# Kernel tuning notes

Measured on AMD Instinct MI355X. Metric: run time of the kernel, lower is better.

The kernel has to match this reference:

```python
import jax, jax.numpy as jnp
import numpy as np
from jax import lax

B, T, EMB = 16384, 50, 16
NS, ND, V = 8, 8, 100000
NEXP = 4
DNN_DIM = ND + NS * EMB + EMB + EMB + EMB  # 184
NEG_INF = float(-2**32 + 1)


def setup_inputs() -> dict:
    key = jax.random.key(0)
    ks = iter(jax.random.split(key, 40))
    def p(shape, s=0.05):
        return jax.random.normal(next(ks), shape, dtype=jnp.float32) * s
    inp = {
        'dense_inputs': jax.random.normal(next(ks), (B, ND), dtype=jnp.float32),
        'sparse_tables': p((NS, V, EMB)),
        'seq_table': p((V, EMB)),
        # DIN attention MLP: input dim 4*EMB = 64
        'att_w1': p((4 * EMB, 64)), 'att_b1': jnp.zeros((64,), jnp.float32),
        'att_w2': p((64, 32)),      'att_b2': jnp.zeros((32,), jnp.float32),
        'att_w3': p((32, 1)),       'att_b3': jnp.zeros((1,), jnp.float32),
        # GRU (reset_after=True, keras default): W [EMB,3H], U [H,3H], b [2,3H]
        'gru_W': p((EMB, 3 * EMB)), 'gru_U': p((EMB, 3 * EMB)),
        'gru_b': jnp.zeros((2, 3 * EMB), jnp.float32),
        # MMOE experts (stacked over expert axis)
        'ew1': p((NEXP, DNN_DIM, 128)), 'eb1': jnp.zeros((NEXP, 128), jnp.float32),
        'ew2': p((NEXP, 128, 64)),      'eb2': jnp.zeros((NEXP, 64), jnp.float32),
        'gfw': p((DNN_DIM, NEXP)), 'gfb': jnp.zeros((NEXP,), jnp.float32),
        'glw': p((DNN_DIM, NEXP)), 'glb': jnp.zeros((NEXP,), jnp.float32),
        'fw': p((64, 1)), 'fb': jnp.zeros((1,), jnp.float32),
        'lw': p((64, 1)), 'lb': jnp.zeros((1,), jnp.float32),
        'sparse_inputs': jax.random.randint(next(ks), (B, NS), 0, V, dtype=jnp.int32),
        'seq_input': jax.random.randint(next(ks), (B, T), 0, V, dtype=jnp.int32),
        'hist_input': jax.random.randint(next(ks), (B, T), 0, V, dtype=jnp.int32),
    }
    return inp


def _din_attention(query, keys, mask, w1, b1, w2, b2, w3, b3):
    # query [B,E], keys [B,T,E], mask [B,T] float (1 valid / 0 pad)
    q = jnp.broadcast_to(query[:, None, :], keys.shape)
    att_in = jnp.concatenate([q, keys, q - keys, q * keys], axis=-1)  # [B,T,4E]
    h = jax.nn.relu(att_in @ w1 + b1)
    h = jax.nn.relu(h @ w2 + b2)
    scores = (h @ w3 + b3)[..., 0]  # [B,T]
    scores = jnp.where(mask > 0, scores, NEG_INF)
    w = jax.nn.softmax(scores, axis=1)
    return jnp.sum(w[..., None] * keys, axis=1)  # [B,E]


def _gru(x, mask_bool, W, U, b):
    # x [B,T,E], mask_bool [B,T]; keras GRU reset_after=True, masked steps keep state
    b_i, b_r = b[0], b[1]
    x_all = x @ W + b_i  # [B,T,3H]
    def step(h, inp):
        x_t, m_t = inp  # [B,3H], [B]
        rec = h @ U + b_r
        xz, xr, xh = jnp.split(x_t, 3, axis=-1)
        rz, rr, rh = jnp.split(rec, 3, axis=-1)
        z = jax.nn.sigmoid(xz + rz)
        r = jax.nn.sigmoid(xr + rr)
        hh = jnp.tanh(xh + r * rh)
        h_new = z * h + (1.0 - z) * hh
        h = jnp.where(m_t[:, None], h_new, h)
        return h, None
    h0 = jnp.zeros((x.shape[0], U.shape[0]), x.dtype)
    h, _ = lax.scan(step, h0, (x_all.transpose(1, 0, 2), mask_bool.T))
    return h  # [B,H]


def reference(dense_inputs, sparse_tables, seq_table,
              att_w1, att_b1, att_w2, att_b2, att_w3, att_b3,
              gru_W, gru_U, gru_b,
              ew1, eb1, ew2, eb2, gfw, gfb, glw, glb, fw, fb, lw, lb,
              sparse_inputs, seq_input, hist_input):
    # sparse embeddings: [B, NS, E]
    sparse_embeds = jax.vmap(lambda t, idx: t[idx], in_axes=(0, 1), out_axes=1)(
        sparse_tables, sparse_inputs)
    sparse_flat = sparse_embeds.reshape(sparse_embeds.shape[0], -1)

    # seq feature: mean pool over time
    seq_flat = jnp.mean(seq_table[seq_input], axis=1)  # [B,E]

    # history: embeds via target item table (s0), DIN attention + GRU
    hist_emb = sparse_tables[0][hist_input]            # [B,T,E]
    mask_f = (hist_input != 0).astype(jnp.float32)
    target_emb = sparse_tables[0][sparse_inputs[:, 0]]  # [B,E]
    din_out = _din_attention(target_emb, hist_emb, mask_f,
                             att_w1, att_b1, att_w2, att_b2, att_w3, att_b3)
    gru_out = _gru(hist_emb, hist_input != 0, gru_W, gru_U, gru_b)

    dnn_input = jnp.concatenate(
        [dense_inputs, sparse_flat, seq_flat, din_out, gru_out], axis=-1)  # [B,184]

    # MMOE experts (dropout is identity at inference)
    h1 = jax.nn.relu(jnp.einsum('bd,edh->beh', dnn_input, ew1) + eb1)
    h2 = jax.nn.relu(jnp.einsum('beh,eho->beo', h1, ew2) + eb2)  # [B,NEXP,64]

    gate_f = jax.nn.softmax(dnn_input @ gfw + gfb, axis=-1)  # [B,NEXP]
    gate_l = jax.nn.softmax(dnn_input @ glw + glb, axis=-1)
    fin_in = jnp.einsum('be,beo->bo', gate_f, h2)
    lik_in = jnp.einsum('be,beo->bo', gate_l, h2)

    finish = jax.nn.sigmoid(fin_in @ fw + fb)  # [B,1]
    like = jax.nn.sigmoid(lik_in @ lw + lb)    # [B,1]
    return finish, like
```

## Files before the change

kernel.cpp:

```cpp
#include <hip/hip_runtime.h>

#define BB 16384
#define TT 50
#define EMBD 16
#define NSP 8
#define NDD 8
#define VV 100000
#define DNN 184
#define NEGINF (-4294967295.0f)

typedef float f32x4 __attribute__((ext_vector_type(4)));
typedef short bf16x8 __attribute__((ext_vector_type(8)));

__device__ __forceinline__ float sigmoidf_(float x) { return 1.0f / (1.0f + __expf(-x)); }
__device__ __forceinline__ float tanhf_(float x) { return 1.0f - 2.0f / (__expf(2.0f * x) + 1.0f); }

__device__ __forceinline__ unsigned short f2bf(float x) {
    union { float f; unsigned u; } c; c.f = x;
    unsigned r = c.u + 0x7FFFu + ((c.u >> 16) & 1u);
    return (unsigned short)(r >> 16);
}
__device__ __forceinline__ unsigned pack2(float lo, float hi) {
    return (unsigned)f2bf(lo) | ((unsigned)f2bf(hi) << 16);
}

__global__ __launch_bounds__(128, 3) void k1_fused(
    const float* __restrict__ dense,
    const float* __restrict__ tables,
    const float* __restrict__ seq_table,
    const float* __restrict__ aw1, const float* __restrict__ ab1,
    const float* __restrict__ aw2, const float* __restrict__ ab2,
    const float* __restrict__ aw3, const float* __restrict__ ab3,
    const float* __restrict__ gW, const float* __restrict__ gU, const float* __restrict__ gB,
    const int* __restrict__ sparse_in, const int* __restrict__ seq_in, const int* __restrict__ hist_in,
    float* __restrict__ dnn_out)
{
    const int w = threadIdx.x >> 6;
    const int lane = threadIdx.x & 63;
    const int b = blockIdx.x * 2 + w;
    const int g = lane >> 4, r16 = lane & 15;

    __shared__ __align__(16) float histE[2][64][16];
    __shared__ float maskL[2][64];
    __shared__ float qsh[2][16];
    __shared__ float dnnL[2][DNN];
    __shared__ float wsoft[2][64];
    __shared__ __align__(16) unsigned short attB[2][64][72];

    if (lane < TT) {
        int hidx = hist_in[b * TT + lane];
        const float4* src = (const float4*)(tables + (size_t)hidx * EMBD);
        float4 a0 = src[0], a1 = src[1], a2 = src[2], a3 = src[3];
        *(float4*)&histE[w][lane][0]  = a0;
        *(float4*)&histE[w][lane][4]  = a1;
        *(float4*)&histE[w][lane][8]  = a2;
        *(float4*)&histE[w][lane][12] = a3;
        maskL[w][lane] = (hidx != 0) ? 1.0f : 0.0f;
    } else {
        float4 z = make_float4(0.f, 0.f, 0.f, 0.f);
        *(float4*)&histE[w][lane][0]  = z;
        *(float4*)&histE[w][lane][4]  = z;
        *(float4*)&histE[w][lane][8]  = z;
        *(float4*)&histE[w][lane][12] = z;
        maskL[w][lane] = 0.0f;
    }
    if (lane < EMBD) {
        int ti = sparse_in[b * NSP];
        qsh[w][lane] = tables[(size_t)ti * EMBD + lane];
    }
    if (lane < NDD) dnnL[w][lane] = dense[b * NDD + lane];
    for (int i = lane; i < NSP * EMBD; i += 64) {
        int s = i >> 4, j = i & 15;
        int idx = sparse_in[b * NSP + s];
        dnnL[w][NDD + i] = tables[((size_t)s * VV + idx) * EMBD + j];
    }
    {
        int gg = lane >> 4, j = lane & 15;
        float acc = 0.0f;
        for (int t = gg; t < TT; t += 4) {
            int idx = seq_in[b * TT + t];
            acc += seq_table[(size_t)idx * EMBD + j];
        }
        acc += __shfl_xor(acc, 16);
        acc += __shfl_xor(acc, 32);
        if (lane < EMBD) dnnL[w][NDD + NSP * EMBD + lane] = acc * (1.0f / TT);
    }
    __syncthreads();

    bf16x8 a1f[4][2];
    #pragma unroll
    for (int mt = 0; mt < 4; ++mt)
        #pragma unroll
        for (int kc = 0; kc < 2; ++kc)
            #pragma unroll
            for (int j = 0; j < 8; ++j)
                a1f[mt][kc][j] = (short)f2bf(aw1[(kc * 32 + g * 8 + j) * 64 + mt * 16 + r16]);
    bf16x8 a2f[2][2];
    #pragma unroll
    for (int mt = 0; mt < 2; ++mt)
        #pragma unroll
        for (int kc = 0; kc < 2; ++kc)
            #pragma unroll
            for (int j = 0; j < 8; ++j)
                a2f[mt][kc][j] = (short)f2bf(aw2[(kc * 32 + g * 8 + j) * 32 + mt * 16 + r16]);

    {
        float qv[16], kv[16];
        #pragma unroll
        for (int j = 0; j < 16; ++j) { qv[j] = qsh[w][j]; kv[j] = histE[w][lane][j]; }
        unsigned short* rowp = &attB[w][lane][0];
        uint4 u;
        u.x = pack2(qv[0], qv[1]);   u.y = pack2(qv[2], qv[3]);
        u.z = pack2(qv[4], qv[5]);   u.w = pack2(qv[6], qv[7]);
        *(uint4*)&rowp[0] = u;
        u.x = pack2(qv[8], qv[9]);   u.y = pack2(qv[10], qv[11]);
        u.z = pack2(qv[12], qv[13]); u.w = pack2(qv[14], qv[15]);
        *(uint4*)&rowp[8] = u;
        u.x = pack2(kv[0], kv[1]);   u.y = pack2(kv[2], kv[3]);
        u.z = pack2(kv[4], kv[5]);   u.w = pack2(kv[6], kv[7]);
        *(uint4*)&rowp[16] = u;
        u.x = pack2(kv[8], kv[9]);   u.y = pack2(kv[10], kv[11]);
        u.z = pack2(kv[12], kv[13]); u.w = pack2(kv[14], kv[15]);
        *(uint4*)&rowp[24] = u;
        u.x = pack2(qv[0]-kv[0], qv[1]-kv[1]);   u.y = pack2(qv[2]-kv[2], qv[3]-kv[3]);
        u.z = pack2(qv[4]-kv[4], qv[5]-kv[5]);   u.w = pack2(qv[6]-kv[6], qv[7]-kv[7]);
        *(uint4*)&rowp[32] = u;
        u.x = pack2(qv[8]-kv[8], qv[9]-kv[9]);   u.y = pack2(qv[10]-kv[10], qv[11]-kv[11]);
        u.z = pack2(qv[12]-kv[12], qv[13]-kv[13]); u.w = pack2(qv[14]-kv[14], qv[15]-kv[15]);
        *(uint4*)&rowp[40] = u;
        u.x = pack2(qv[0]*kv[0], qv[1]*kv[1]);   u.y = pack2(qv[2]*kv[2], qv[3]*kv[3]);
        u.z = pack2(qv[4]*kv[4], qv[5]*kv[5]);   u.w = pack2(qv[6]*kv[6], qv[7]*kv[7]);
        *(uint4*)&rowp[48] = u;
        u.x = pack2(qv[8]*kv[8], qv[9]*kv[9]);   u.y = pack2(qv[10]*kv[10], qv[11]*kv[11]);
        u.z = pack2(qv[12]*kv[12], qv[13]*kv[13]); u.w = pack2(qv[14]*kv[14], qv[15]*kv[15]);
        *(uint4*)&rowp[56] = u;
    }
    __syncthreads();

    #pragma unroll
    for (int nt = 0; nt < 4; ++nt) {
        const unsigned short* rp = &attB[w][nt * 16 + r16][g * 8];
        bf16x8 b0 = *(const bf16x8*)(rp);
        bf16x8 b1 = *(const bf16x8*)(rp + 32);
        #pragma unroll
        for (int mt = 0; mt < 4; ++mt) {
            f32x4 acc = {0.f, 0.f, 0.f, 0.f};
            acc = __builtin_amdgcn_mfma_f32_16x16x32_bf16(a1f[mt][0], b0, acc, 0, 0, 0);
            acc = __builtin_amdgcn_mfma_f32_16x16x32_bf16(a1f[mt][1], b1, acc, 0, 0, 0);
            const float4 bia = *(const float4*)(ab1 + mt * 16 + g * 4);
            float v0 = fmaxf(acc[0] + bia.x, 0.0f);
            float v1 = fmaxf(acc[1] + bia.y, 0.0f);
            float v2 = fmaxf(acc[2] + bia.z, 0.0f);
            float v3 = fmaxf(acc[3] + bia.w, 0.0f);
            uint2 pw; pw.x = pack2(v0, v1); pw.y = pack2(v2, v3);
            *(uint2*)&attB[w][nt * 16 + r16][mt * 16 + g * 4] = pw;
        }
    }

    float snt[4];
    #pragma unroll
    for (int nt = 0; nt < 4; ++nt) {
        const unsigned short* rp = &attB[w][nt * 16 + r16][g * 8];
        bf16x8 c0 = *(const bf16x8*)(rp);
        bf16x8 c1 = *(const bf16x8*)(rp + 32);
        float sp = 0.0f;
        #pragma unroll
        for (int mt = 0; mt < 2; ++mt) {
            f32x4 acc = {0.f, 0.f, 0.f, 0.f};
            acc = __builtin_amdgcn_mfma_f32_16x16x32_bf16(a2f[mt][0], c0, acc, 0, 0, 0);
            acc = __builtin_amdgcn_mfma_f32_16x16x32_bf16(a2f[mt][1], c1, acc, 0, 0, 0);
            const float4 bia = *(const float4*)(ab2 + mt * 16 + g * 4);
            const float4 w3v = *(const float4*)(aw3 + mt * 16 + g * 4);
            sp += fmaxf(acc[0] + bia.x, 0.0f) * w3v.x;
            sp += fmaxf(acc[1] + bia.y, 0.0f) * w3v.y;
            sp += fmaxf(acc[2] + bia.z, 0.0f) * w3v.z;
            sp += fmaxf(acc[3] + bia.w, 0.0f) * w3v.w;
        }
        sp += __shfl_xor(sp, 16);
        sp += __shfl_xor(sp, 32);
        snt[nt] = sp;
    }
    float score = (g == 0) ? snt[0] : (g == 1) ? snt[1] : (g == 2) ? snt[2] : snt[3];
    score += ab3[0];

    float mask = maskL[w][lane];
    score = (lane < TT && mask > 0.0f) ? score : NEGINF;
    float m = score;
    #pragma unroll
    for (int off = 32; off > 0; off >>= 1) m = fmaxf(m, __shfl_xor(m, off));
    float e = (lane < TT) ? __expf(score - m) : 0.0f;
    float ssum = e;
    #pragma unroll
    for (int off = 32; off > 0; off >>= 1) ssum += __shfl_xor(ssum, off);
    wsoft[w][lane] = e / ssum;
    __syncthreads();

    {
        float da = 0.0f;
        for (int t = g; t < TT; t += 4) da += wsoft[w][t] * histE[w][t][r16];
        da += __shfl_xor(da, 16);
        da += __shfl_xor(da, 32);
        if (lane < EMBD) dnnL[w][NDD + NSP * EMBD + EMBD + lane] = da;
    }

    float Wc[EMBD], Uc[EMBD], bi = 0.0f, br = 0.0f;
    if (lane < 48) {
        #pragma unroll
        for (int v = 0; v < EMBD; ++v) { Wc[v] = gW[v * 48 + lane]; Uc[v] = gU[v * 48 + lane]; }
        bi = gB[lane]; br = gB[48 + lane];
    }
    float hcur = 0.0f;
    for (int t = 0; t < TT; ++t) {
        float4 x0 = *(const float4*)&histE[w][t][0];
        float4 x1 = *(const float4*)&histE[w][t][4];
        float4 x2 = *(const float4*)&histE[w][t][8];
        float4 x3 = *(const float4*)&histE[w][t][12];
        float mt = maskL[w][t];
        float hv[16];
        #pragma unroll
        for (int v = 0; v < 16; ++v) hv[v] = __shfl(hcur, v);
        float xa = bi, rc = br;
        xa += x0.x*Wc[0] + x0.y*Wc[1] + x0.z*Wc[2] + x0.w*Wc[3];
        xa += x1.x*Wc[4] + x1.y*Wc[5] + x1.z*Wc[6] + x1.w*Wc[7];
        xa += x2.x*Wc[8] + x2.y*Wc[9] + x2.z*Wc[10] + x2.w*Wc[11];
        xa += x3.x*Wc[12] + x3.y*Wc[13] + x3.z*Wc[14] + x3.w*Wc[15];
        #pragma unroll
        for (int v = 0; v < 16; ++v) rc += hv[v] * Uc[v];
        float xr = __shfl(xa, lane + 16), xh = __shfl(xa, lane + 32);
        float rr = __shfl(rc, lane + 16), rh = __shfl(rc, lane + 32);
        float z  = sigmoidf_(xa + rc);
        float r  = sigmoidf_(xr + rr);
        float hh = tanhf_(xh + r * rh);
        float hnew = z * hcur + (1.0f - z) * hh;
        hcur = (mt > 0.0f) ? hnew : hcur;
    }
    if (lane < EMBD) dnnL[w][DNN - EMBD + lane] = hcur;
    __syncthreads();

    for (int i = lane; i < DNN; i += 64)
        dnn_out[(size_t)b * DNN + i] = dnnL[w][i];
}

#define BBT 8
__global__ __launch_bounds__(256) void k2_mmoe(
    const float* __restrict__ dnn_in,
    const float* __restrict__ ew1, const float* __restrict__ eb1,
    const float* __restrict__ ew2, const float* __restrict__ eb2,
    const float* __restrict__ gfw, const float* __restrict__ gfb,
    const float* __restrict__ glw, const float* __restrict__ glb,
    const float* __restrict__ fw, const float* __restrict__ fb,
    const float* __restrict__ lw, const float* __restrict__ lb,
    float* __restrict__ out)
{
    const int tid = threadIdx.x;
    const int b0 = blockIdx.x * BBT;

    __shared__ float dlds[BBT * DNN];
    __shared__ float h1L[BBT][512];
    __shared__ float h2L[BBT][256];
    __shared__ float gateL[BBT][8];

    {
        const float* drow = dnn_in + (size_t)b0 * DNN;
        for (int i = tid; i < BBT * DNN; i += 256) dlds[i] = drow[i];
    }
    __syncthreads();

    {
        int col0 = tid;
        int e0 = col0 >> 7, i0 = col0 & 127;
        const float* wp0 = ew1 + (size_t)e0 * DNN * 128 + i0;
        const float* wp1 = ew1 + (size_t)(e0 + 2) * DNN * 128 + i0;
        float acc0[BBT], acc1[BBT];
        float bias0 = eb1[col0], bias1 = eb1[col0 + 256];
        #pragma unroll
        for (int bb = 0; bb < BBT; ++bb) { acc0[bb] = bias0; acc1[bb] = bias1; }
        for (int d = 0; d < DNN; d += 4) {
            float w00 = wp0[(size_t)(d + 0) * 128], w01 = wp0[(size_t)(d + 1) * 128];
            float w02 = wp0[(size_t)(d + 2) * 128], w03 = wp0[(size_t)(d + 3) * 128];
            float w10 = wp1[(size_t)(d + 0) * 128], w11 = wp1[(size_t)(d + 1) * 128];
            float w12 = wp1[(size_t)(d + 2) * 128], w13 = wp1[(size_t)(d + 3) * 128];
            #pragma unroll
            for (int bb = 0; bb < BBT; ++bb) {
                const float4 h4 = *(const float4*)&dlds[bb * DNN + d];
                acc0[bb] += h4.x * w00 + h4.y * w01 + h4.z * w02 + h4.w * w03;
                acc1[bb] += h4.x * w10 + h4.y * w11 + h4.z * w12 + h4.w * w13;
            }
        }
        #pragma unroll
        for (int bb = 0; bb < BBT; ++bb) {
            h1L[bb][col0]       = fmaxf(acc0[bb], 0.0f);
            h1L[bb][col0 + 256] = fmaxf(acc1[bb], 0.0f);
        }
    }

    if (tid < 64) {
        int bb = tid >> 3, which = (tid >> 2) & 1, eidx = tid & 3;
        const float* gw = which ? glw : gfw;
        float acc = which ? glb[eidx] : gfb[eidx];
        for (int d = 0; d < DNN; ++d) acc += dlds[bb * DNN + d] * gw[d * 4 + eidx];
        gateL[bb][which * 4 + eidx] = acc;
    }
    __syncthreads();

    if (tid < 16) {
        int bb = tid >> 1, which = tid & 1;
        float l0 = gateL[bb][which * 4 + 0], l1 = gateL[bb][which * 4 + 1];
        float l2 = gateL[bb][which * 4 + 2], l3 = gateL[bb][which * 4 + 3];
        float mm = fmaxf(fmaxf(l0, l1), fmaxf(l2, l3));
        float e0 = __expf(l0 - mm), e1 = __expf(l1 - mm), e2 = __expf(l2 - mm), e3 = __expf(l3 - mm);
        float ss = e0 + e1 + e2 + e3;
        gateL[bb][which * 4 + 0] = e0 / ss; gateL[bb][which * 4 + 1] = e1 / ss;
        gateL[bb][which * 4 + 2] = e2 / ss; gateL[bb][which * 4 + 3] = e3 / ss;
    }

    {
        int col = tid;
        int eidx = col >> 6, i = col & 63;
        const float* wp = ew2 + (size_t)eidx * 128 * 64 + i;
        float acc[BBT];
        float bias = eb2[col];
        #pragma unroll
        for (int bb = 0; bb < BBT; ++bb) acc[bb] = bias;
        for (int d = 0; d < 128; d += 4) {
            float w0 = wp[(d + 0) * 64], w1v = wp[(d + 1) * 64];
            float w2v = wp[(d + 2) * 64], w3v = wp[(d + 3) * 64];
            #pragma unroll
            for (int bb = 0; bb < BBT; ++bb) {
                const float4 h4 = *(const float4*)&h1L[bb][eidx * 128 + d];
                acc[bb] += h4.x * w0 + h4.y * w1v + h4.z * w2v + h4.w * w3v;
            }
        }
        #pragma unroll
        for (int bb = 0; bb < BBT; ++bb) h2L[bb][col] = fmaxf(acc[bb], 0.0f);
    }
    __syncthreads();

    {
        int wv = tid >> 6, lane = tid & 63;
        for (int it = 0; it < 2; ++it) {
            int bb = wv * 2 + it;
            float h0 = h2L[bb][lane], h1v = h2L[bb][64 + lane];
            float h2v = h2L[bb][128 + lane], h3v = h2L[bb][192 + lane];
            float fin = gateL[bb][0] * h0 + gateL[bb][1] * h1v + gateL[bb][2] * h2v + gateL[bb][3] * h3v;
            float lik = gateL[bb][4] * h0 + gateL[bb][5] * h1v + gateL[bb][6] * h2v + gateL[bb][7] * h3v;
            float pf = fin * fw[lane];
            float pl = lik * lw[lane];
            #pragma unroll
            for (int off = 32; off > 0; off >>= 1) {
                pf += __shfl_xor(pf, off);
                pl += __shfl_xor(pl, off);
            }
            if (lane == 0) {
                out[b0 + bb]      = sigmoidf_(pf + fb[0]);
                out[BB + b0 + bb] = sigmoidf_(pl + lb[0]);
            }
        }
    }
}

extern "C" void kernel_launch(void* const* d_in, const int* in_sizes, int n_in,
                              void* d_out, int out_size, void* d_ws, size_t ws_size,
                              hipStream_t stream)
{
    const float* dense     = (const float*)d_in[0];
    const float* tables    = (const float*)d_in[1];
    const float* seq_table = (const float*)d_in[2];
    const float* aw1 = (const float*)d_in[3];  const float* ab1 = (const float*)d_in[4];
    const float* aw2 = (const float*)d_in[5];  const float* ab2 = (const float*)d_in[6];
    const float* aw3 = (const float*)d_in[7];  const float* ab3 = (const float*)d_in[8];
    const float* gW  = (const float*)d_in[9];  const float* gU  = (const float*)d_in[10];
    const float* gB  = (const float*)d_in[11];
    const float* ew1 = (const float*)d_in[12]; const float* eb1 = (const float*)d_in[13];
    const float* ew2 = (const float*)d_in[14]; const float* eb2 = (const float*)d_in[15];
    const float* gfw = (const float*)d_in[16]; const float* gfb = (const float*)d_in[17];
    const float* glw = (const float*)d_in[18]; const float* glb = (const float*)d_in[19];
    const float* fw  = (const float*)d_in[20]; const float* fb  = (const float*)d_in[21];
    const float* lw  = (const float*)d_in[22]; const float* lb  = (const float*)d_in[23];
    const int* sparse_in = (const int*)d_in[24];
    const int* seq_in    = (const int*)d_in[25];
    const int* hist_in   = (const int*)d_in[26];
    float* out = (float*)d_out;
    float* dnn_ws = (float*)d_ws;

    hipLaunchKernelGGL(k1_fused, dim3(BB / 2), dim3(128), 0, stream,
                       dense, tables, seq_table, aw1, ab1, aw2, ab2, aw3, ab3,
                       gW, gU, gB, sparse_in, seq_in, hist_in, dnn_ws);
    hipLaunchKernelGGL(k2_mmoe, dim3(BB / BBT), dim3(256), 0, stream,
                       dnn_ws, ew1, eb1, ew2, eb2, gfw, gfb, glw, glb,
                       fw, fb, lw, lb, out);
}
```

Before: 528.5 us.

## Rewrite MMOE expert stage with bf16 MFMA and pre-transposed weights

```diff
diff --git a/kernel.cpp b/kernel.cpp
--- a/kernel.cpp
+++ b/kernel.cpp
@@ -22,6 +22,22 @@
 }
 __device__ __forceinline__ unsigned pack2(float lo, float hi) {
     return (unsigned)f2bf(lo) | ((unsigned)f2bf(hi) << 16);
+}
+
+__global__ __launch_bounds__(192) void kconv(
+    const float* __restrict__ ew1, const float* __restrict__ ew2,
+    unsigned short* __restrict__ w1t, unsigned short* __restrict__ w2t)
+{
+    const int bid = blockIdx.x, tid = threadIdx.x;
+    if (bid < 512) {
+        float v = 0.0f;
+        if (tid < 184) v = ew1[(size_t)(bid >> 7) * 184 * 128 + (size_t)tid * 128 + (bid & 127)];
+        w1t[bid * 192 + tid] = f2bf(v);
+    } else {
+        const int e = (bid - 512) >> 6, n2 = (bid - 512) & 63;
+        if (tid < 128)
+            w2t[(size_t)(e * 64 + n2) * 128 + tid] = f2bf(ew2[(size_t)e * 128 * 64 + tid * 64 + n2]);
+    }
 }
 
 __global__ __launch_bounds__(128, 3) void k1_fused(
@@ -241,11 +257,11 @@
         dnn_out[(size_t)b * DNN + i] = dnnL[w][i];
 }
 
-#define BBT 8
-__global__ __launch_bounds__(256) void k2_mmoe(
+#define K2B 32
+__global__ __launch_bounds__(256) void k2_mfma(
     const float* __restrict__ dnn_in,
-    const float* __restrict__ ew1, const float* __restrict__ eb1,
-    const float* __restrict__ ew2, const float* __restrict__ eb2,
+    const unsigned short* __restrict__ w1t, const unsigned short* __restrict__ w2t,
+    const float* __restrict__ eb1, const float* __restrict__ eb2,
     const float* __restrict__ gfw, const float* __restrict__ gfb,
     const float* __restrict__ glw, const float* __restrict__ glb,
     const float* __restrict__ fw, const float* __restrict__ fb,
@@ -253,109 +269,123 @@
     float* __restrict__ out)
 {
     const int tid = threadIdx.x;
-    const int b0 = blockIdx.x * BBT;
-
-    __shared__ float dlds[BBT * DNN];
-    __shared__ float h1L[BBT][512];
-    __shared__ float h2L[BBT][256];
-    __shared__ float gateL[BBT][8];
-
-    {
-        const float* drow = dnn_in + (size_t)b0 * DNN;
-        for (int i = tid; i < BBT * DNN; i += 256) dlds[i] = drow[i];
-    }
-    __syncthreads();
-
-    {
-        int col0 = tid;
-        int e0 = col0 >> 7, i0 = col0 & 127;
-        const float* wp0 = ew1 + (size_t)e0 * DNN * 128 + i0;
-        const float* wp1 = ew1 + (size_t)(e0 + 2) * DNN * 128 + i0;
-        float acc0[BBT], acc1[BBT];
-        float bias0 = eb1[col0], bias1 = eb1[col0 + 256];
-        #pragma unroll
-        for (int bb = 0; bb < BBT; ++bb) { acc0[bb] = bias0; acc1[bb] = bias1; }
-        for (int d = 0; d < DNN; d += 4) {
-            float w00 = wp0[(size_t)(d + 0) * 128], w01 = wp0[(size_t)(d + 1) * 128];
-            float w02 = wp0[(size_t)(d + 2) * 128], w03 = wp0[(size_t)(d + 3) * 128];
-            float w10 = wp1[(size_t)(d + 0) * 128], w11 = wp1[(size_t)(d + 1) * 128];
-            float w12 = wp1[(size_t)(d + 2) * 128], w13 = wp1[(size_t)(d + 3) * 128];
-            #pragma unroll
-            for (int bb = 0; bb < BBT; ++bb) {
-                const float4 h4 = *(const float4*)&dlds[bb * DNN + d];
-                acc0[bb] += h4.x * w00 + h4.y * w01 + h4.z * w02 + h4.w * w03;
-                acc1[bb] += h4.x * w10 + h4.y * w11 + h4.z * w12 + h4.w * w13;
+    const int b0 = blockIdx.x * K2B;
+    const int wv = tid >> 6, lane = tid & 63, g = lane >> 4, r16 = lane & 15;
+    const int rt = wv >> 1, nh = wv & 1;
+
+    __shared__ __align__(16) unsigned short dldsb[K2B][208];
+    __shared__ __align__(16) unsigned short h1b[K2B][520];
+    __shared__ float gateL[K2B][8];
+    __shared__ float part[2][2][16][2];
+
+    {
+        const int row = tid >> 3, c8 = tid & 7;
+        const float* src = dnn_in + (size_t)(b0 + row) * DNN + c8 * 23;
+        unsigned short* dst = &dldsb[row][c8 * 23];
+        #pragma unroll
+        for (int c = 0; c < 23; ++c) dst[c] = f2bf(src[c]);
+        #pragma unroll
+        for (int c = 0; c < 3; ++c) dldsb[row][184 + c8 * 3 + c] = 0;
+    }
+    {
+        const int bb = tid >> 3, which = (tid >> 2) & 1, e = tid & 3;
+        const float* gw = which ? glw : gfw;
+        float acc = which ? glb[e] : gfb[e];
+        const float* dr = dnn_in + (size_t)(b0 + bb) * DNN;
+        for (int d = 0; d < DNN; ++d) acc += dr[d] * gw[d * 4 + e];
+        gateL[bb][which * 4 + e] = acc;
+    }
+    __syncthreads();
+
+    if (tid < 64) {
+        const int bb = tid >> 1, which = tid & 1;
+        float l0 = gateL[bb][which*4+0], l1 = gateL[bb][which*4+1];
+        float l2 = gateL[bb][which*4+2], l3 = gateL[bb][which*4+3];
+        float mm = fmaxf(fmaxf(l0, l1), fmaxf(l2, l3));
+        float e0 = __expf(l0-mm), e1 = __expf(l1-mm), e2 = __expf(l2-mm), e3 = __expf(l3-mm);
+        float ss = e0 + e1 + e2 + e3;
+        gateL[bb][which*4+0] = e0/ss; gateL[bb][which*4+1] = e1/ss;
+        gateL[bb][which*4+2] = e2/ss; gateL[bb][which*4+3] = e3/ss;
+    }
+
+    {
+        bf16x8 af[6];
+        #pragma unroll
+        for (int kk = 0; kk < 6; ++kk)
+            af[kk] = *(const bf16x8*)&dldsb[rt * 16 + r16][kk * 32 + g * 8];
+        for (int nt = nh * 16; nt < nh * 16 + 16; ++nt) {
+            f32x4 acc = {0.f, 0.f, 0.f, 0.f};
+            const unsigned short* wp = w1t + (size_t)(nt * 16 + r16) * 192 + g * 8;
+            #pragma unroll
+            for (int kk = 0; kk < 6; ++kk) {
+                bf16x8 bf = *(const bf16x8*)(wp + kk * 32);
+                acc = __builtin_amdgcn_mfma_f32_16x16x32_bf16(af[kk], bf, acc, 0, 0, 0);
             }
-        }
-        #pragma unroll
-        for (int bb = 0; bb < BBT; ++bb) {
-            h1L[bb][col0]       = fmaxf(acc0[bb], 0.0f);
-            h1L[bb][col0 + 256] = fmaxf(acc1[bb], 0.0f);
-        }
-    }
+            const float eb1v = eb1[nt * 16 + r16];
+            #pragma unroll
+            for (int reg = 0; reg < 4; ++reg)
+                h1b[rt * 16 + g * 4 + reg][nt * 16 + r16] = f2bf(fmaxf(acc[reg] + eb1v, 0.0f));
+        }
+    }
+    __syncthreads();
+
+    {
+        float accF[4] = {0.f,0.f,0.f,0.f}, accL[4] = {0.f,0.f,0.f,0.f};
+        #pragma unroll
+        for (int eh = 0; eh < 2; ++eh) {
+            const int e = nh * 2 + eh;
+            bf16x8 af2[4];
+            #pragma unroll
+            for (int kk = 0; kk < 4; ++kk)
+                af2[kk] = *(const bf16x8*)&h1b[rt * 16 + r16][e * 128 + kk * 32 + g * 8];
+            float gF[4], gL[4];
+            #pragma unroll
+            for (int reg = 0; reg < 4; ++reg) {
+                gF[reg] = gateL[rt * 16 + g * 4 + reg][e];
+                gL[reg] = gateL[rt * 16 + g * 4 + reg][4 + e];
+            }
+            #pragma unroll
+            for (int i16 = 0; i16 < 4; ++i16) {
+                f32x4 acc = {0.f, 0.f, 0.f, 0.f};
+                const unsigned short* wp = w2t + (size_t)(e * 64 + i16 * 16 + r16) * 128 + g * 8;
+                #pragma unroll
+                for (int kk = 0; kk < 4; ++kk) {
+                    bf16x8 bf = *(const bf16x8*)(wp + kk * 32);
+                    acc = __builtin_amdgcn_mfma_f32_16x16x32_bf16(af2[kk], bf, acc, 0, 0, 0);
+                }
+                const float eb2v = eb2[e * 64 + i16 * 16 + r16];
+                const float fwv = fw[i16 * 16 + r16], lwv = lw[i16 * 16 + r16];
+                #pragma unroll
+                for (int reg = 0; reg < 4; ++reg) {
+                    float h2v = fmaxf(acc[reg] + eb2v, 0.0f);
+                    accF[reg] += gF[reg] * h2v * fwv;
+                    accL[reg] += gL[reg] * h2v * lwv;
+                }
+            }
+        }
+        #pragma unroll
+        for (int off = 1; off < 16; off <<= 1) {
+            #pragma unroll
+            for (int reg = 0; reg < 4; ++reg) {
+                accF[reg] += __shfl_xor(accF[reg], off);
+                accL[reg] += __shfl_xor(accL[reg], off);
+            }
+        }
+        if (r16 == 0) {
+            #pragma unroll
+            for (int reg = 0; reg < 4; ++reg) {
+                part[rt][nh][g * 4 + reg][0] = accF[reg];
+                part[rt][nh][g * 4 + reg][1] = accL[reg];
+            }
+        }
+    }
+    __syncthreads();
 
     if (tid < 64) {
-        int bb = tid >> 3, which = (tid >> 2) & 1, eidx = tid & 3;
-        const float* gw = which ? glw : gfw;
-        float acc = which ? glb[eidx] : gfb[eidx];
-        for (int d = 0; d < DNN; ++d) acc += dlds[bb * DNN + d] * gw[d * 4 + eidx];
-        gateL[bb][which * 4 + eidx] = acc;
-    }
-    __syncthreads();
-
-    if (tid < 16) {
-        int bb = tid >> 1, which = tid & 1;
-        float l0 = gateL[bb][which * 4 + 0], l1 = gateL[bb][which * 4 + 1];
-        float l2 = gateL[bb][which * 4 + 2], l3 = gateL[bb][which * 4 + 3];
-        float mm = fmaxf(fmaxf(l0, l1), fmaxf(l2, l3));
-        float e0 = __expf(l0 - mm), e1 = __expf(l1 - mm), e2 = __expf(l2 - mm), e3 = __expf(l3 - mm);
-        float ss = e0 + e1 + e2 + e3;
-        gateL[bb][which * 4 + 0] = e0 / ss; gateL[bb][which * 4 + 1] = e1 / ss;
-        gateL[bb][which * 4 + 2] = e2 / ss; gateL[bb][which * 4 + 3] = e3 / ss;
-    }
-
-    {
-        int col = tid;
-        int eidx = col >> 6, i = col & 63;
-        const float* wp = ew2 + (size_t)eidx * 128 * 64 + i;
-        float acc[BBT];
-        float bias = eb2[col];
-        #pragma unroll
-        for (int bb = 0; bb < BBT; ++bb) acc[bb] = bias;
-        for (int d = 0; d < 128; d += 4) {
-            float w0 = wp[(d + 0) * 64], w1v = wp[(d + 1) * 64];
-            float w2v = wp[(d + 2) * 64], w3v = wp[(d + 3) * 64];
-            #pragma unroll
-            for (int bb = 0; bb < BBT; ++bb) {
-                const float4 h4 = *(const float4*)&h1L[bb][eidx * 128 + d];
-                acc[bb] += h4.x * w0 + h4.y * w1v + h4.z * w2v + h4.w * w3v;
-            }
-        }
-        #pragma unroll
-        for (int bb = 0; bb < BBT; ++bb) h2L[bb][col] = fmaxf(acc[bb], 0.0f);
-    }
-    __syncthreads();
-
-    {
-        int wv = tid >> 6, lane = tid & 63;
-        for (int it = 0; it < 2; ++it) {
-            int bb = wv * 2 + it;
-            float h0 = h2L[bb][lane], h1v = h2L[bb][64 + lane];
-            float h2v = h2L[bb][128 + lane], h3v = h2L[bb][192 + lane];
-            float fin = gateL[bb][0] * h0 + gateL[bb][1] * h1v + gateL[bb][2] * h2v + gateL[bb][3] * h3v;
-            float lik = gateL[bb][4] * h0 + gateL[bb][5] * h1v + gateL[bb][6] * h2v + gateL[bb][7] * h3v;
-            float pf = fin * fw[lane];
-            float pl = lik * lw[lane];
-            #pragma unroll
-            for (int off = 32; off > 0; off >>= 1) {
-                pf += __shfl_xor(pf, off);
-                pl += __shfl_xor(pl, off);
-            }
-            if (lane == 0) {
-                out[b0 + bb]      = sigmoidf_(pf + fb[0]);
-                out[BB + b0 + bb] = sigmoidf_(pl + lb[0]);
-            }
-        }
+        const int bl = tid & 31, head = tid >> 5;
+        float v = part[bl >> 4][0][bl & 15][head] + part[bl >> 4][1][bl & 15][head];
+        if (head == 0) out[b0 + bl]      = sigmoidf_(v + fb[0]);
+        else           out[BB + b0 + bl] = sigmoidf_(v + lb[0]);
     }
 }
 
@@ -381,12 +411,16 @@
     const int* seq_in    = (const int*)d_in[25];
     const int* hist_in   = (const int*)d_in[26];
     float* out = (float*)d_out;
+
     float* dnn_ws = (float*)d_ws;
-
+    unsigned short* w1t = (unsigned short*)((char*)d_ws + (size_t)BB * DNN * 4);
+    unsigned short* w2t = w1t + 512 * 192;
+
+    hipLaunchKernelGGL(kconv, dim3(512 + 256), dim3(192), 0, stream, ew1, ew2, w1t, w2t);
     hipLaunchKernelGGL(k1_fused, dim3(BB / 2), dim3(128), 0, stream,
                        dense, tables, seq_table, aw1, ab1, aw2, ab2, aw3, ab3,
                        gW, gU, gB, sparse_in, seq_in, hist_in, dnn_ws);
-    hipLaunchKernelGGL(k2_mmoe, dim3(BB / BBT), dim3(256), 0, stream,
-                       dnn_ws, ew1, eb1, ew2, eb2, gfw, gfb, glw, glb,
+    hipLaunchKernelGGL(k2_mfma, dim3(BB / K2B), dim3(256), 0, stream,
+                       dnn_ws, w1t, w2t, eb1, eb2, gfw, gfb, glw, glb,
                        fw, fb, lw, lb, out);
 }
```

After: 478.2 us. 1.11x faster.
